# Optimization experiments

Hardware: AMD Instinct MI355X
Metric: run time of the kernel (lower is better)

The kernel has to match this reference:

```python
import jax, jax.numpy as jnp
import numpy as np

B, S, HID = 2, 1024, 4096
NH, NKV, D = 32, 8, 128
G = NH // NKV            # query heads per KV head (GQA group size)
WINDOW = 512             # sliding window
ROPE_BASE = 10000.0
NEG = -1e30


def setup_inputs() -> dict:
    key = jax.random.key(0)
    k0, k1, k2, k3, k4 = jax.random.split(key, 5)
    hidden_states = jax.random.normal(k0, (B, S, HID), jnp.float32)
    # rotate-half RoPE tables, width = head_dim
    inv_freq = 1.0 / (ROPE_BASE ** (jnp.arange(0, D, 2, dtype=jnp.float32) / D))
    freqs = jnp.outer(jnp.arange(S, dtype=jnp.float32), inv_freq)
    emb = jnp.concatenate([freqs, freqs], axis=-1)  # [S, D]
    cos, sin = jnp.cos(emb), jnp.sin(emb)
    qkv_out = (NH + 2 * NKV) * D  # fused QKV: 6144
    w_qkv = jax.random.normal(k1, (qkv_out, HID), jnp.float32) / np.sqrt(HID).astype(np.float32)
    b_qkv = jax.random.normal(k2, (qkv_out,), jnp.float32) * 0.01
    w_o = jax.random.normal(k3, (HID, NH * D), jnp.float32) / np.sqrt(NH * D).astype(np.float32)
    b_o = jax.random.normal(k4, (HID,), jnp.float32) * 0.01
    return dict(hidden_states=hidden_states, cos=cos, sin=sin,
                w_qkv=w_qkv, b_qkv=b_qkv, w_o=w_o, b_o=b_o)


def _rotate_half(x):
    x1, x2 = jnp.split(x, 2, axis=-1)
    return jnp.concatenate([-x2, x1], axis=-1)


def reference(hidden_states, cos, sin, w_qkv, b_qkv, w_o, b_o):
    # fused QKV projection (with bias, per attention_bias=True)
    qkv = jnp.einsum('bsh,oh->bso', hidden_states, w_qkv) + b_qkv
    q = qkv[..., : NH * D].reshape(B, S, NKV, G, D)
    k = qkv[..., NH * D : (NH + NKV) * D].reshape(B, S, NKV, D)
    v = qkv[..., (NH + NKV) * D :].reshape(B, S, NKV, D)
    # rotate-half RoPE
    c = cos[None, :, None, :]  # [1,S,1,D]
    s = sin[None, :, None, :]
    q = q * c[..., None, :] + _rotate_half(q) * s[..., None, :]
    k = k * c + _rotate_half(k) * s
    # GQA attention: scores [B, NKV, G, Sq, Sk]
    scores = jnp.einsum('bqkgd,bskd->bkgqs', q, k) / np.sqrt(D).astype(np.float32)
    i = jnp.arange(S)[:, None]
    j = jnp.arange(S)[None, :]
    mask = (j <= i) & (i - j < WINDOW)  # causal + sliding window
    scores = jnp.where(mask, scores, NEG)
    p = jax.nn.softmax(scores, axis=-1)
    attn = jnp.einsum('bkgqs,bskd->bqkgd', p, v).reshape(B, S, NH * D)
    return jnp.einsum('bsd,hd->bsh', attn, w_o) + b_o
```

## Files before the change

### kernel.cpp

```cpp
#include <hip/hip_runtime.h>
#include <hip/hip_bf16.h>

#define B_      2
#define S_      1024
#define HID     4096
#define NH      32
#define NKV     8
#define D_      128
#define G_      4
#define WINDOW  512
#define QKV_OUT 6144
#define M_TOT   2048
#define CH      32
#define VSTR    40

typedef __bf16 bf16x8 __attribute__((ext_vector_type(8)));
typedef float  f32x4  __attribute__((ext_vector_type(4)));
typedef unsigned short u16x8 __attribute__((ext_vector_type(8)));

#define AS1 __attribute__((address_space(1)))
#define AS3 __attribute__((address_space(3)))

static __device__ __forceinline__ float bf2f(unsigned short u) {
    union { unsigned int i; float f; } v; v.i = ((unsigned int)u) << 16; return v.f;
}
static __device__ __forceinline__ unsigned short f2bf(float f) {
    union { float f; unsigned int i; } v; v.f = f;
    unsigned int x = v.i;
    return (unsigned short)((x + 0x7fffu + ((x >> 16) & 1u)) >> 16);
}
static __device__ __forceinline__ void gl2lds16(const void* g, void* l) {
    __builtin_amdgcn_global_load_lds((const AS1 void*)g, (AS3 void*)l, 16, 0, 0);
}

__global__ __launch_bounds__(256)
void conv_f32_bf16(const float* __restrict__ src, unsigned short* __restrict__ dst, int n8)
{
    int i = blockIdx.x * 256 + threadIdx.x;
    if (i >= n8) return;
    const float* p = src + (size_t)i * 8;
    float4 f0 = *(const float4*)p;
    float4 f1 = *(const float4*)(p + 4);
    u16x8 h;
    h[0]=f2bf(f0.x); h[1]=f2bf(f0.y); h[2]=f2bf(f0.z); h[3]=f2bf(f0.w);
    h[4]=f2bf(f1.x); h[5]=f2bf(f1.y); h[6]=f2bf(f1.z); h[7]=f2bf(f1.w);
    *(u16x8*)&dst[(size_t)i * 8] = h;
}

#define PHASE_TAIL(MT0, MT1)                                                           \
    __builtin_amdgcn_sched_barrier(0);                                                 \
    __builtin_amdgcn_s_barrier();                                                      \
    asm volatile("s_waitcnt lgkmcnt(0)" ::: "memory");                                 \
    __builtin_amdgcn_sched_barrier(0);                                                 \
    __builtin_amdgcn_s_setprio(1);                                                     \
    _Pragma("unroll")                                                                  \
    for (int nt = 0; nt < 4; ++nt) {                                                   \
        acc[MT0][nt] = __builtin_amdgcn_mfma_f32_16x16x32_bf16(a0[0], b[nt][0], acc[MT0][nt], 0, 0, 0); \
        acc[MT0][nt] = __builtin_amdgcn_mfma_f32_16x16x32_bf16(a0[1], b[nt][1], acc[MT0][nt], 0, 0, 0); \
        acc[MT1][nt] = __builtin_amdgcn_mfma_f32_16x16x32_bf16(a1[0], b[nt][0], acc[MT1][nt], 0, 0, 0); \
        acc[MT1][nt] = __builtin_amdgcn_mfma_f32_16x16x32_bf16(a1[1], b[nt][1], acc[MT1][nt], 0, 0, 0); \
    }                                                                                  \
    __builtin_amdgcn_s_setprio(0);

template<bool C_BF16>
__global__ __launch_bounds__(512, 2)
void gemm256_8ph(const unsigned short* __restrict__ A,
                 const unsigned short* __restrict__ Bw,
                 const float* __restrict__ bias,
                 void* __restrict__ Cv,
                 int M, int N, int K)
{
    __shared__ __attribute__((aligned(1024))) unsigned short lds[65536];

    const int tid  = threadIdx.x;
    const int lane = tid & 63;
    const int w    = tid >> 6;
    const int m_   = w >> 2;
    const int n_   = w & 3;
    const int lm   = lane & 15, quad = lane >> 4;
    const int m0   = blockIdx.y * 256, n0 = blockIdx.x * 256;
    const int nkt  = K >> 6;

    const int srow = lane >> 3;
    const int scol = ((lane & 7) ^ srow) * 8;

    const int arow0 = m0 + m_ * 128 + n_ * 16;
    const int arow1 = arow0 + 64;
    const int brow  = n0 + w * 32;

    const int ldsAr = m_ * 8192;
    const int ldsA0 = ldsAr + n_ * 1024;
    const int ldsA1 = ldsA0 + 4096;
    const int ldsBs = 32768 + m_ * 8192 + n_ * 2048;
    const int ldsBr = 32768 + (n_ >> 1) * 8192 + (n_ & 1) * 4096;

    f32x4 acc[8][4] = {};

    auto stA = [&](int T, int rp) {
        const int k0   = T << 6;
        const int bufo = (T & 1) << 14;
        const int rb   = (rp ? arow1 : arow0) + srow;
        const int lb   = (rp ? ldsA1 : ldsA0) + bufo + lane * 8;
        gl2lds16(&A[(size_t)rb * K + k0 + scol],       &lds[lb]);
        gl2lds16(&A[(size_t)(rb + 8) * K + k0 + scol], &lds[lb + 512]);
    };
    auto stB = [&](int T, int pr) {
        const int k0   = T << 6;
        const int bufo = (T & 1) << 14;
        const int rb   = brow + pr * 16 + srow;
        const int lb   = ldsBs + pr * 1024 + bufo + lane * 8;
        gl2lds16(&Bw[(size_t)rb * K + k0 + scol],       &lds[lb]);
        gl2lds16(&Bw[(size_t)(rb + 8) * K + k0 + scol], &lds[lb + 512]);
    };
    auto rdA = [&](int bufo, int mt, int ks) -> bf16x8 {
        int e = (mt * 16 + lm) * 64 + ks * 32 + quad * 8;
        e ^= ((e >> 6) & 7) << 3;
        return *(const bf16x8*)&lds[bufo + ldsAr + e];
    };
    auto rdB = [&](int bufo, int nt, int ks) -> bf16x8 {
        int e = (nt * 16 + lm) * 64 + ks * 32 + quad * 8;
        e ^= ((e >> 6) & 7) << 3;
        return *(const bf16x8*)&lds[bufo + ldsBr + e];
    };

    stB(0, 0); stB(0, 1); stA(0, 0); stA(0, 1);
    stB(1, 0); stB(1, 1); stA(1, 0);
    asm volatile("s_waitcnt vmcnt(6)" ::: "memory");
    __builtin_amdgcn_sched_barrier(0);
    __builtin_amdgcn_s_barrier();

    #pragma unroll 1
    for (int i = 0; i < nkt; ++i) {
        const int bufo = (i & 1) << 14;
        bf16x8 b[4][2];
        {
            bf16x8 a0[2], a1[2];
            #pragma unroll
            for (int ks = 0; ks < 2; ++ks) { a0[ks] = rdA(bufo, 0, ks); a1[ks] = rdA(bufo, 1, ks); }
            #pragma unroll
            for (int nt = 0; nt < 4; ++nt)
                #pragma unroll
                for (int ks = 0; ks < 2; ++ks) b[nt][ks] = rdB(bufo, nt, ks);
            if (i + 1 < nkt) stA(i + 1, 1);
            __builtin_amdgcn_sched_barrier(0);
            asm volatile("s_waitcnt lgkmcnt(8)" ::: "memory");
            PHASE_TAIL(0, 1)
            __builtin_amdgcn_sched_barrier(0);
            __builtin_amdgcn_s_barrier();
        }
        {
            bf16x8 a0[2], a1[2];
            #pragma unroll
            for (int ks = 0; ks < 2; ++ks) { a0[ks] = rdA(bufo, 2, ks); a1[ks] = rdA(bufo, 3, ks); }
            if (i + 2 < nkt) stB(i + 2, 0);
            PHASE_TAIL(2, 3)
            __builtin_amdgcn_sched_barrier(0);
            __builtin_amdgcn_s_barrier();
        }
        {
            bf16x8 a0[2], a1[2];
            #pragma unroll
            for (int ks = 0; ks < 2; ++ks) { a0[ks] = rdA(bufo, 4, ks); a1[ks] = rdA(bufo, 5, ks); }
            if (i + 2 < nkt) stB(i + 2, 1);
            PHASE_TAIL(4, 5)
            __builtin_amdgcn_sched_barrier(0);
            __builtin_amdgcn_s_barrier();
        }
        {
            bf16x8 a0[2], a1[2];
            #pragma unroll
            for (int ks = 0; ks < 2; ++ks) { a0[ks] = rdA(bufo, 6, ks); a1[ks] = rdA(bufo, 7, ks); }
            if (i + 2 < nkt) stA(i + 2, 0);
            PHASE_TAIL(6, 7)
            __builtin_amdgcn_sched_barrier(0);
            if (i < nkt - 2)       { asm volatile("s_waitcnt vmcnt(6)" ::: "memory"); }
            else if (i == nkt - 2) { asm volatile("s_waitcnt vmcnt(0)" ::: "memory"); }
            __builtin_amdgcn_sched_barrier(0);
            __builtin_amdgcn_s_barrier();
        }
    }

    #pragma unroll
    for (int nt = 0; nt < 4; ++nt) {
        const int col = n0 + n_ * 64 + nt * 16 + lm;
        const float bv = bias[col];
        #pragma unroll
        for (int mt = 0; mt < 8; ++mt) {
            const int rowb = m0 + m_ * 128 + mt * 16 + quad * 4;
            #pragma unroll
            for (int r = 0; r < 4; ++r) {
                const float val = acc[mt][nt][r] + bv;
                if (C_BF16)
                    ((unsigned short*)Cv)[(size_t)(rowb + r) * N + col] = f2bf(val);
                else
                    ((float*)Cv)[(size_t)(rowb + r) * N + col] = val;
            }
        }
    }
}

template<bool C_BF16>
__global__ __launch_bounds__(256)
void gemm_bf16_bt(const unsigned short* __restrict__ A,
                  const unsigned short* __restrict__ Bw,
                  const float* __restrict__ bias,
                  void* __restrict__ Cv,
                  int M, int N, int K)
{
    __shared__ unsigned short As[128 * 32];
    __shared__ unsigned short Bs[128 * 32];

    const int tid  = threadIdx.x;
    const int m0   = blockIdx.y * 128;
    const int n0   = blockIdx.x * 128;
    const int wave = tid >> 6, lane = tid & 63;
    const int wm   = (wave >> 1) * 64;
    const int wn   = (wave & 1) * 64;
    const int lm   = lane & 15, quad = lane >> 4;

    f32x4 acc[4][4] = {};

    for (int k0 = 0; k0 < K; k0 += 32) {
        __syncthreads();
        #pragma unroll
        for (int p = 0; p < 2; ++p) {
            int chunk = tid + p * 256;
            int row   = chunk >> 2;
            int off   = (chunk & 3) * 8;
            gl2lds16(&A [(size_t)(m0 + row) * K + k0 + off], &As[chunk * 8]);
            gl2lds16(&Bw[(size_t)(n0 + row) * K + k0 + off], &Bs[chunk * 8]);
        }
        __syncthreads();

        bf16x8 afr[4], bfr[4];
        #pragma unroll
        for (int i = 0; i < 4; ++i)
            afr[i] = *(const bf16x8*)&As[(wm + i * 16 + lm) * 32 + quad * 8];
        #pragma unroll
        for (int j = 0; j < 4; ++j)
            bfr[j] = *(const bf16x8*)&Bs[(wn + j * 16 + lm) * 32 + quad * 8];

        #pragma unroll
        for (int i = 0; i < 4; ++i)
            #pragma unroll
            for (int j = 0; j < 4; ++j)
                acc[i][j] = __builtin_amdgcn_mfma_f32_16x16x32_bf16(afr[i], bfr[j], acc[i][j], 0, 0, 0);
    }

    #pragma unroll
    for (int j = 0; j < 4; ++j) {
        int col = n0 + wn + j * 16 + lm;
        float bv = bias[col];
        #pragma unroll
        for (int i = 0; i < 4; ++i) {
            int rowb = m0 + wm + i * 16 + quad * 4;
            #pragma unroll
            for (int r = 0; r < 4; ++r) {
                float val = acc[i][j][r] + bv;
                if (C_BF16)
                    ((unsigned short*)Cv)[(size_t)(rowb + r) * N + col] = f2bf(val);
                else
                    ((float*)Cv)[(size_t)(rowb + r) * N + col] = val;
            }
        }
    }
}

template<bool A_BF16, bool C_BF16>
__global__ __launch_bounds__(256)
void gemm_bt_bias(const void* __restrict__ Av,
                  const float* __restrict__ Bw,
                  const float* __restrict__ bias,
                  void* __restrict__ Cv,
                  int M, int N, int K)
{
    __shared__ unsigned short As[128 * 40];
    __shared__ unsigned short Bs[128 * 40];

    const int tid  = threadIdx.x;
    const int m0   = blockIdx.y * 128;
    const int n0   = blockIdx.x * 128;
    const int wave = tid >> 6, lane = tid & 63;
    const int wm   = (wave >> 1) * 64;
    const int wn   = (wave & 1) * 64;
    const int lm   = lane & 15, quad = lane >> 4;

    f32x4 acc[4][4] = {};

    for (int k0 = 0; k0 < K; k0 += 32) {
        __syncthreads();
        #pragma unroll
        for (int c = 0; c < 2; ++c) {
            int chunk = tid + c * 256;
            int row   = chunk >> 2;
            int off   = (chunk & 3) * 8;
            if (A_BF16) {
                *(u16x8*)&As[row * 40 + off] =
                    *(const u16x8*)&((const unsigned short*)Av)[(size_t)(m0 + row) * K + k0 + off];
            } else {
                const float* ap = &((const float*)Av)[(size_t)(m0 + row) * K + k0 + off];
                float4 f0 = *(const float4*)ap;
                float4 f1 = *(const float4*)(ap + 4);
                u16x8 h;
                h[0]=f2bf(f0.x); h[1]=f2bf(f0.y); h[2]=f2bf(f0.z); h[3]=f2bf(f0.w);
                h[4]=f2bf(f1.x); h[5]=f2bf(f1.y); h[6]=f2bf(f1.z); h[7]=f2bf(f1.w);
                *(u16x8*)&As[row * 40 + off] = h;
            }
            {
                const float* bp = &Bw[(size_t)(n0 + row) * K + k0 + off];
                float4 f0 = *(const float4*)bp;
                float4 f1 = *(const float4*)(bp + 4);
                u16x8 h;
                h[0]=f2bf(f0.x); h[1]=f2bf(f0.y); h[2]=f2bf(f0.z); h[3]=f2bf(f0.w);
                h[4]=f2bf(f1.x); h[5]=f2bf(f1.y); h[6]=f2bf(f1.z); h[7]=f2bf(f1.w);
                *(u16x8*)&Bs[row * 40 + off] = h;
            }
        }
        __syncthreads();

        bf16x8 afr[4], bfr[4];
        #pragma unroll
        for (int i = 0; i < 4; ++i)
            afr[i] = *(const bf16x8*)&As[(wm + i * 16 + lm) * 40 + quad * 8];
        #pragma unroll
        for (int j = 0; j < 4; ++j)
            bfr[j] = *(const bf16x8*)&Bs[(wn + j * 16 + lm) * 40 + quad * 8];

        #pragma unroll
        for (int i = 0; i < 4; ++i)
            #pragma unroll
            for (int j = 0; j < 4; ++j)
                acc[i][j] = __builtin_amdgcn_mfma_f32_16x16x32_bf16(afr[i], bfr[j], acc[i][j], 0, 0, 0);
    }

    #pragma unroll
    for (int j = 0; j < 4; ++j) {
        int col = n0 + wn + j * 16 + lm;
        float bv = bias[col];
        #pragma unroll
        for (int i = 0; i < 4; ++i) {
            int rowb = m0 + wm + i * 16 + quad * 4;
            #pragma unroll
            for (int r = 0; r < 4; ++r) {
                float val = acc[i][j][r] + bv;
                if (C_BF16)
                    ((unsigned short*)Cv)[(size_t)(rowb + r) * N + col] = f2bf(val);
                else
                    ((float*)Cv)[(size_t)(rowb + r) * N + col] = val;
            }
        }
    }
}

__global__ __launch_bounds__(256)
void rope_kernel(unsigned short* __restrict__ qkv,
                 const float* __restrict__ cosb,
                 const float* __restrict__ sinb)
{
    int t    = blockIdx.x * 256 + threadIdx.x;
    int d    = t & 63;
    int rest = t >> 6;
    int head = rest % 40;
    int m    = rest / 40;
    int s    = m & (S_ - 1);
    int obase = (head < NH) ? head * D_ : HID + (head - NH) * D_;
    size_t base = (size_t)m * QKV_OUT + obase;

    float x1 = bf2f(qkv[base + d]);
    float x2 = bf2f(qkv[base + d + 64]);
    float c1 = cosb[s * D_ + d];
    float s1 = sinb[s * D_ + d];
    float c2 = cosb[s * D_ + d + 64];
    float s2 = sinb[s * D_ + d + 64];
    qkv[base + d]      = f2bf(x1 * c1 - x2 * s1);
    qkv[base + d + 64] = f2bf(x2 * c2 + x1 * s2);
}

__global__ __launch_bounds__(256)
void attn_mfma(const unsigned short* __restrict__ qkv,
               unsigned short* __restrict__ attn)
{
    __shared__ unsigned short Kl[CH * 136];
    __shared__ unsigned short Vt[128 * VSTR];
    __shared__ unsigned short Pl[4][16 * 40];

    const int tid  = threadIdx.x;
    const int wave = tid >> 6, lane = tid & 63;
    const int lm   = lane & 15, quad = lane >> 4;
    const int h    = blockIdx.y;
    const int b    = blockIdx.z;
    const int kvh  = h >> 2;
    const int r0b  = blockIdx.x * 64;
    const int rw0  = r0b + wave * 16;

    const size_t qkv_b = (size_t)b * S_ * QKV_OUT;
    const float SCL = 0.12751974f;

    bf16x8 qf[4];
    {
        const unsigned short* qrow = qkv + qkv_b + (size_t)(rw0 + lm) * QKV_OUT + h * D_ + quad * 8;
        #pragma unroll
        for (int kb = 0; kb < 4; ++kb)
            qf[kb] = *(const bf16x8*)(qrow + kb * 32);
    }

    f32x4 O[8] = {};
    float mrow[4] = {-1e30f, -1e30f, -1e30f, -1e30f};
    float lrow[4] = {0.f, 0.f, 0.f, 0.f};

    const int c0   = max(0, r0b - (WINDOW - 1)) & ~(CH - 1);
    const int cend = r0b + 64 - CH;

    for (int c = c0; c <= cend; c += CH) {
        __syncthreads();
        #pragma unroll
        for (int p = 0; p < 2; ++p) {
            int idx = tid + p * 256;
            int row = idx >> 4;
            int d0  = (idx & 15) * 8;
            *(u16x8*)&Kl[row * 136 + d0] =
                *(const u16x8*)(qkv + qkv_b + (size_t)(c + row) * QKV_OUT + HID + kvh * D_ + d0);
        }
        {
            int r2 = (tid & 15) * 2;
            int d0 = (tid >> 4) * 8;
            const unsigned short* vg = qkv + qkv_b + (size_t)(c + r2) * QKV_OUT + HID + NKV * D_ + kvh * D_ + d0;
            u16x8 va = *(const u16x8*)vg;
            u16x8 vb = *(const u16x8*)(vg + QKV_OUT);
            #pragma unroll
            for (int e = 0; e < 8; ++e) {
                unsigned int pack = (unsigned int)va[e] | ((unsigned int)vb[e] << 16);
                *(unsigned int*)&Vt[(d0 + e) * VSTR + r2] = pack;
            }
        }
        __syncthreads();

        if (c + CH - 1 < rw0 - (WINDOW - 1) || c > rw0 + 15) continue;

        f32x4 s0 = {}, s1 = {};
        #pragma unroll
        for (int kb = 0; kb < 4; ++kb) {
            bf16x8 b0 = *(const bf16x8*)&Kl[lm * 136 + kb * 32 + quad * 8];
            bf16x8 b1 = *(const bf16x8*)&Kl[(16 + lm) * 136 + kb * 32 + quad * 8];
            s0 = __builtin_amdgcn_mfma_f32_16x16x32_bf16(qf[kb], b0, s0, 0, 0, 0);
            s1 = __builtin_amdgcn_mfma_f32_16x16x32_bf16(qf[kb], b1, s1, 0, 0, 0);
        }

        const int j0 = c + lm, j1 = c + 16 + lm;
        float alpha[4];
        #pragma unroll
        for (int r = 0; r < 4; ++r) {
            int row = rw0 + quad * 4 + r;
            float t0 = (j0 <= row && row - j0 < WINDOW) ? s0[r] : -3.0e38f;
            float t1 = (j1 <= row && row - j1 < WINDOW) ? s1[r] : -3.0e38f;
            float cm = fmaxf(t0, t1);
            #pragma unroll
            for (int o = 8; o >= 1; o >>= 1) cm = fmaxf(cm, __shfl_xor(cm, o, 16));
            float mnew = fmaxf(mrow[r], cm);
            float al   = exp2f((mrow[r] - mnew) * SCL);
            float p0   = exp2f((t0 - mnew) * SCL);
            float p1   = exp2f((t1 - mnew) * SCL);
            float rs   = p0 + p1;
            #pragma unroll
            for (int o = 8; o >= 1; o >>= 1) rs += __shfl_xor(rs, o, 16);
            mrow[r] = mnew;
            lrow[r] = lrow[r] * al + rs;
            alpha[r] = al;
            Pl[wave][(quad * 4 + r) * 40 + lm]      = f2bf(p0);
            Pl[wave][(quad * 4 + r) * 40 + 16 + lm] = f2bf(p1);
        }

        #pragma unroll
        for (int nt = 0; nt < 8; ++nt)
            #pragma unroll
            for (int r = 0; r < 4; ++r)
                O[nt][r] *= alpha[r];

        bf16x8 pa = *(const bf16x8*)&Pl[wave][lm * 40 + quad * 8];
        #pragma unroll
        for (int nt = 0; nt < 8; ++nt) {
            bf16x8 vbf = *(const bf16x8*)&Vt[(nt * 16 + lm) * VSTR + quad * 8];
            O[nt] = __builtin_amdgcn_mfma_f32_16x16x32_bf16(pa, vbf, O[nt], 0, 0, 0);
        }
    }

    float il[4];
    #pragma unroll
    for (int r = 0; r < 4; ++r) il[r] = 1.0f / lrow[r];
    #pragma unroll
    for (int nt = 0; nt < 8; ++nt)
        #pragma unroll
        for (int r = 0; r < 4; ++r) {
            int row = rw0 + quad * 4 + r;
            attn[(size_t)(b * S_ + row) * (NH * D_) + h * D_ + nt * 16 + lm] = f2bf(O[nt][r] * il[r]);
        }
}

extern "C" void kernel_launch(void* const* d_in, const int* in_sizes, int n_in,
                              void* d_out, int out_size, void* d_ws, size_t ws_size,
                              hipStream_t stream)
{
    const float* hidden = (const float*)d_in[0];
    const float* cosb   = (const float*)d_in[1];
    const float* sinb   = (const float*)d_in[2];
    const float* w_qkv  = (const float*)d_in[3];
    const float* b_qkv  = (const float*)d_in[4];
    const float* w_o    = (const float*)d_in[5];
    const float* b_o    = (const float*)d_in[6];
    float* out = (float*)d_out;

    unsigned char* ws = (unsigned char*)d_ws;
    const size_t QKV_B  = (size_t)M_TOT * QKV_OUT * 2;
    const size_t ATTN_B = (size_t)M_TOT * HID * 2;
    const size_t HB_B   = (size_t)M_TOT * HID * 2;
    const size_t WQ_B   = (size_t)QKV_OUT * HID * 2;
    const size_t WO_B   = (size_t)HID * HID * 2;
    const size_t NEED   = QKV_B + ATTN_B + HB_B + WQ_B;

    unsigned short* qkv_ws  = (unsigned short*)(ws);
    unsigned short* attn_ws = (unsigned short*)(ws + QKV_B);

    dim3 blk(256);

    if (ws_size >= NEED && WO_B <= HB_B + WQ_B) {
        unsigned short* hb = (unsigned short*)(ws + QKV_B + ATTN_B);
        unsigned short* wq = (unsigned short*)(ws + QKV_B + ATTN_B + HB_B);
        unsigned short* wo = (unsigned short*)(ws + QKV_B + ATTN_B);

        int n8h = M_TOT * HID / 8;
        int n8q = QKV_OUT * HID / 8;
        int n8o = HID * HID / 8;
        conv_f32_bf16<<<dim3((n8h + 255) / 256), blk, 0, stream>>>(hidden, hb, n8h);
        conv_f32_bf16<<<dim3((n8q + 255) / 256), blk, 0, stream>>>(w_qkv, wq, n8q);
        gemm256_8ph<true><<<dim3(QKV_OUT / 256, M_TOT / 256), dim3(512), 0, stream>>>(
            hb, wq, b_qkv, qkv_ws, M_TOT, QKV_OUT, HID);
        rope_kernel<<<dim3((M_TOT * 40 * 64) / 256), blk, 0, stream>>>(qkv_ws, cosb, sinb);
        conv_f32_bf16<<<dim3((n8o + 255) / 256), blk, 0, stream>>>(w_o, wo, n8o);
        attn_mfma<<<dim3(S_ / 64, NH, B_), blk, 0, stream>>>(qkv_ws, attn_ws);
        gemm_bf16_bt<false><<<dim3(HID / 128, M_TOT / 128), blk, 0, stream>>>(
            attn_ws, wo, b_o, out, M_TOT, HID, NH * D_);
    } else {
        gemm_bt_bias<false, true><<<dim3(QKV_OUT / 128, M_TOT / 128), blk, 0, stream>>>(
            hidden, w_qkv, b_qkv, qkv_ws, M_TOT, QKV_OUT, HID);
        rope_kernel<<<dim3((M_TOT * 40 * 64) / 256), blk, 0, stream>>>(qkv_ws, cosb, sinb);
        attn_mfma<<<dim3(S_ / 64, NH, B_), blk, 0, stream>>>(qkv_ws, attn_ws);
        gemm_bt_bias<true, false><<<dim3(HID / 128, M_TOT / 128), blk, 0, stream>>>(
            attn_ws, w_o, b_o, out, M_TOT, HID, NH * D_);
    }
}
```

Measured before the change: 541.9 us.

## Software-pipeline LDS fragment reads one phase ahead of MFMAs in GEMM

Restructures the 8-phase GEMM main loop so that the A fragments for the next phase and the B/A fragments for the next k-tile are read from LDS while the current phase's MFMAs execute. Register double-buffering (aP/aQ, bC) and partial lgkmcnt waits replace the previous read-then-wait-then-compute pattern, which had an extra barrier per phase. The goal is to hide LDS latency behind matrix-core work and drop barriers, at the cost of higher VGPR pressure and tighter correctness constraints around buffer reuse.

```diff
diff --git a/kernel.cpp b/kernel.cpp
--- a/kernel.cpp
+++ b/kernel.cpp
@@ -47,20 +47,20 @@
     *(u16x8*)&dst[(size_t)i * 8] = h;
 }
 
-#define PHASE_TAIL(MT0, MT1)                                                           \
-    __builtin_amdgcn_sched_barrier(0);                                                 \
-    __builtin_amdgcn_s_barrier();                                                      \
-    asm volatile("s_waitcnt lgkmcnt(0)" ::: "memory");                                 \
-    __builtin_amdgcn_sched_barrier(0);                                                 \
-    __builtin_amdgcn_s_setprio(1);                                                     \
+#define MFMA_PAIR(MT0, MT1, AR)                                                        \
+    __builtin_amdgcn_s_setprio(1);                                                    \
     _Pragma("unroll")                                                                  \
     for (int nt = 0; nt < 4; ++nt) {                                                   \
-        acc[MT0][nt] = __builtin_amdgcn_mfma_f32_16x16x32_bf16(a0[0], b[nt][0], acc[MT0][nt], 0, 0, 0); \
-        acc[MT0][nt] = __builtin_amdgcn_mfma_f32_16x16x32_bf16(a0[1], b[nt][1], acc[MT0][nt], 0, 0, 0); \
-        acc[MT1][nt] = __builtin_amdgcn_mfma_f32_16x16x32_bf16(a1[0], b[nt][0], acc[MT1][nt], 0, 0, 0); \
-        acc[MT1][nt] = __builtin_amdgcn_mfma_f32_16x16x32_bf16(a1[1], b[nt][1], acc[MT1][nt], 0, 0, 0); \
+        acc[MT0][nt] = __builtin_amdgcn_mfma_f32_16x16x32_bf16(AR[0][0], bC[nt][0], acc[MT0][nt], 0, 0, 0); \
+        acc[MT0][nt] = __builtin_amdgcn_mfma_f32_16x16x32_bf16(AR[0][1], bC[nt][1], acc[MT0][nt], 0, 0, 0); \
+        acc[MT1][nt] = __builtin_amdgcn_mfma_f32_16x16x32_bf16(AR[1][0], bC[nt][0], acc[MT1][nt], 0, 0, 0); \
+        acc[MT1][nt] = __builtin_amdgcn_mfma_f32_16x16x32_bf16(AR[1][1], bC[nt][1], acc[MT1][nt], 0, 0, 0); \
     }                                                                                  \
     __builtin_amdgcn_s_setprio(0);
+
+#define SCHED __builtin_amdgcn_sched_barrier(0)
+#define WAITLGKM(N) do { asm volatile("s_waitcnt lgkmcnt(" #N ")" ::: "memory"); SCHED; } while (0)
+#define BARRIER do { SCHED; __builtin_amdgcn_s_barrier(); SCHED; } while (0)
 
 template<bool C_BF16>
 __global__ __launch_bounds__(512, 2)
@@ -95,6 +95,8 @@
     const int ldsBr = 32768 + (n_ >> 1) * 8192 + (n_ & 1) * 4096;
 
     f32x4 acc[8][4] = {};
+    bf16x8 bC[4][2];
+    bf16x8 aP[2][2], aQ[2][2];
 
     auto stA = [&](int T, int rp) {
         const int k0   = T << 6;
@@ -122,62 +124,57 @@
         e ^= ((e >> 6) & 7) << 3;
         return *(const bf16x8*)&lds[bufo + ldsBr + e];
     };
+    auto rdBoundary = [&](int T) {
+        const int bufo = (T & 1) << 14;
+        #pragma unroll
+        for (int nt = 0; nt < 4; ++nt)
+            #pragma unroll
+            for (int ks = 0; ks < 2; ++ks) bC[nt][ks] = rdB(bufo, nt, ks);
+        #pragma unroll
+        for (int ks = 0; ks < 2; ++ks) { aP[0][ks] = rdA(bufo, 0, ks); aP[1][ks] = rdA(bufo, 1, ks); }
+    };
 
     stB(0, 0); stB(0, 1); stA(0, 0); stA(0, 1);
     stB(1, 0); stB(1, 1); stA(1, 0);
     asm volatile("s_waitcnt vmcnt(6)" ::: "memory");
-    __builtin_amdgcn_sched_barrier(0);
-    __builtin_amdgcn_s_barrier();
+    BARRIER;
+    rdBoundary(0);
+    SCHED;
 
     #pragma unroll 1
     for (int i = 0; i < nkt; ++i) {
         const int bufo = (i & 1) << 14;
-        bf16x8 b[4][2];
-        {
-            bf16x8 a0[2], a1[2];
-            #pragma unroll
-            for (int ks = 0; ks < 2; ++ks) { a0[ks] = rdA(bufo, 0, ks); a1[ks] = rdA(bufo, 1, ks); }
-            #pragma unroll
-            for (int nt = 0; nt < 4; ++nt)
-                #pragma unroll
-                for (int ks = 0; ks < 2; ++ks) b[nt][ks] = rdB(bufo, nt, ks);
-            if (i + 1 < nkt) stA(i + 1, 1);
-            __builtin_amdgcn_sched_barrier(0);
-            asm volatile("s_waitcnt lgkmcnt(8)" ::: "memory");
-            PHASE_TAIL(0, 1)
-            __builtin_amdgcn_sched_barrier(0);
-            __builtin_amdgcn_s_barrier();
-        }
-        {
-            bf16x8 a0[2], a1[2];
-            #pragma unroll
-            for (int ks = 0; ks < 2; ++ks) { a0[ks] = rdA(bufo, 2, ks); a1[ks] = rdA(bufo, 3, ks); }
-            if (i + 2 < nkt) stB(i + 2, 0);
-            PHASE_TAIL(2, 3)
-            __builtin_amdgcn_sched_barrier(0);
-            __builtin_amdgcn_s_barrier();
-        }
-        {
-            bf16x8 a0[2], a1[2];
-            #pragma unroll
-            for (int ks = 0; ks < 2; ++ks) { a0[ks] = rdA(bufo, 4, ks); a1[ks] = rdA(bufo, 5, ks); }
-            if (i + 2 < nkt) stB(i + 2, 1);
-            PHASE_TAIL(4, 5)
-            __builtin_amdgcn_sched_barrier(0);
-            __builtin_amdgcn_s_barrier();
-        }
-        {
-            bf16x8 a0[2], a1[2];
-            #pragma unroll
-            for (int ks = 0; ks < 2; ++ks) { a0[ks] = rdA(bufo, 6, ks); a1[ks] = rdA(bufo, 7, ks); }
-            if (i + 2 < nkt) stA(i + 2, 0);
-            PHASE_TAIL(6, 7)
-            __builtin_amdgcn_sched_barrier(0);
-            if (i < nkt - 2)       { asm volatile("s_waitcnt vmcnt(6)" ::: "memory"); }
-            else if (i == nkt - 2) { asm volatile("s_waitcnt vmcnt(0)" ::: "memory"); }
-            __builtin_amdgcn_sched_barrier(0);
-            __builtin_amdgcn_s_barrier();
-        }
+        if (i + 1 < nkt) stA(i + 1, 1);
+        #pragma unroll
+        for (int ks = 0; ks < 2; ++ks) { aQ[0][ks] = rdA(bufo, 2, ks); aQ[1][ks] = rdA(bufo, 3, ks); }
+        SCHED;
+        WAITLGKM(4);
+        MFMA_PAIR(0, 1, aP)
+        BARRIER;
+        if (i + 2 < nkt) stB(i + 2, 0);
+        #pragma unroll
+        for (int ks = 0; ks < 2; ++ks) { aP[0][ks] = rdA(bufo, 4, ks); aP[1][ks] = rdA(bufo, 5, ks); }
+        SCHED;
+        WAITLGKM(4);
+        MFMA_PAIR(2, 3, aQ)
+        BARRIER;
+        if (i + 2 < nkt) stB(i + 2, 1);
+        #pragma unroll
+        for (int ks = 0; ks < 2; ++ks) { aQ[0][ks] = rdA(bufo, 6, ks); aQ[1][ks] = rdA(bufo, 7, ks); }
+        SCHED;
+        WAITLGKM(4);
+        MFMA_PAIR(4, 5, aP)
+        BARRIER;
+        if (i + 2 < nkt) stA(i + 2, 0);
+        SCHED;
+        WAITLGKM(0);
+        MFMA_PAIR(6, 7, aQ)
+        SCHED;
+        if (i + 2 < nkt)      { asm volatile("s_waitcnt vmcnt(6)" ::: "memory"); }
+        else if (i + 1 < nkt) { asm volatile("s_waitcnt vmcnt(0)" ::: "memory"); }
+        BARRIER;
+        if (i + 1 < nkt) rdBoundary(i + 1);
+        SCHED;
     }
 
     #pragma unroll
```

Result: no change. 538.2 us (-0.7%).
